# Kernel tuning notes

Measured on AMD Instinct MI355X. Metric: run time of the kernel, lower is better.

Reference implementation:

```python
import jax, jax.numpy as jnp
import numpy as np

RADIUS = 2  # scipy grey_opening 'size' -> flat 2x2 structuring element


def _grey_opening_2d(x, w=RADIUS):
    """Channel-wise grey opening matching scipy.ndimage.grey_opening(slice, size=w).

    scipy semantics for even size w=2:
      erosion window at i covers {i-1, i}  (filter centered, left-heavy)
      dilation window at i covers {i, i+1} (structuring element reflected)
    boundary mode 'reflect' in scipy.ndimage repeats the edge sample, which is
    jnp.pad mode='symmetric'.
    x: [B, C, H, W]
    """
    lo = w // 2          # left/top pad for erosion (=1 for w=2)
    hi = w - 1 - lo      # right/bottom pad for erosion (=0 for w=2)
    win = (1, 1, w, w)
    strides = (1, 1, 1, 1)
    # erosion: sliding-window min
    xe = jnp.pad(x, ((0, 0), (0, 0), (lo, hi), (lo, hi)), mode='symmetric')
    er = jax.lax.reduce_window(xe, jnp.array(jnp.inf, x.dtype), jax.lax.min,
                               win, strides, 'VALID')
    # dilation: sliding-window max with reflected (right-heavy) window
    xd = jnp.pad(er, ((0, 0), (0, 0), (hi, lo), (hi, lo)), mode='symmetric')
    return jax.lax.reduce_window(xd, jnp.array(-jnp.inf, x.dtype), jax.lax.max,
                                 win, strides, 'VALID')


def setup_inputs() -> dict:
    key = jax.random.key(0)
    labels = jax.random.uniform(key, (8, 16, 512, 512), dtype=jnp.float32)
    return {"labels": labels}


def reference(labels):
    # smooth labels are detached in the original (numpy round-trip + .detach())
    smooth = jax.lax.stop_gradient(_grey_opening_2d(labels))
    return jnp.mean((labels - smooth) ** 2)
```

## Files before the change

kernel.cpp:

```cpp
#include <hip/hip_runtime.h>


#define BLK 256
#define GRID 2048

__global__ __launch_bounds__(BLK) void opening_partial_kernel(
    const float* __restrict__ x, float* __restrict__ partial, int nGroups)
{
    float acc = 0.f;
    const int stride = gridDim.x * blockDim.x;
    for (int g = blockIdx.x * blockDim.x + threadIdx.x; g < nGroups; g += stride) {
        const int j = (g & 127) << 2;
        const int i = (g >> 7) & 511;
        const long long planeOff = ((long long)(g >> 16)) << 18;
        const float* r1 = x + planeOff + ((long long)i << 9);
        const float* r0 = (i > 0)   ? r1 - 512 : r1;
        const float* r2 = (i < 511) ? r1 + 512 : r1;

        const float4 v0 = *(const float4*)(r0 + j);
        const float4 v1 = *(const float4*)(r1 + j);
        const float4 v2 = *(const float4*)(r2 + j);
        const int jm = (j > 0)   ? j - 1 : 0;
        const int jp = (j < 508) ? j + 4 : 511;
        const float a0 = r0[jm], e0 = r0[jp];
        const float a1 = r1[jm], e1 = r1[jp];
        const float a2 = r2[jm], e2 = r2[jp];

        float m0[5] = { fminf(a0, v0.x), fminf(v0.x, v0.y), fminf(v0.y, v0.z),
                        fminf(v0.z, v0.w), fminf(v0.w, e0) };
        float m1[5] = { fminf(a1, v1.x), fminf(v1.x, v1.y), fminf(v1.y, v1.z),
                        fminf(v1.z, v1.w), fminf(v1.w, e1) };
        float m2[5] = { fminf(a2, v2.x), fminf(v2.x, v2.y), fminf(v2.y, v2.z),
                        fminf(v2.z, v2.w), fminf(v2.w, e2) };

        float erA[5], erB[5];
        const bool notBottom = (i < 511);
        #pragma unroll
        for (int c = 0; c < 5; ++c) {
            erA[c] = fminf(m0[c], m1[c]);
            const float inner = notBottom ? m1[c] : m0[c];
            erB[c] = fminf(inner, m2[c]);
        }

        const bool lastChunk = (j == 508);
        const float xv[4] = { v1.x, v1.y, v1.z, v1.w };
        #pragma unroll
        for (int k = 0; k < 4; ++k) {
            float eA2 = erA[k + 1], eB2 = erB[k + 1];
            if (lastChunk && k == 3) { eA2 = erA[3]; eB2 = erB[3]; }
            const float dl = fmaxf(fmaxf(erA[k], eA2), fmaxf(erB[k], eB2));
            const float d = xv[k] - dl;
            acc = fmaf(d, d, acc);
        }
    }

    #pragma unroll
    for (int off = 32; off > 0; off >>= 1)
        acc += __shfl_down(acc, off, 64);
    __shared__ float s[BLK / 64];
    if ((threadIdx.x & 63) == 0) s[threadIdx.x >> 6] = acc;
    __syncthreads();
    if (threadIdx.x == 0) {
        float t = 0.f;
        #pragma unroll
        for (int w = 0; w < BLK / 64; ++w) t += s[w];
        partial[blockIdx.x] = t;
    }
}

__global__ __launch_bounds__(256) void final_reduce_kernel(
    const float* __restrict__ partial, float* __restrict__ out, int n, float invN)
{
    float acc = 0.f;
    for (int idx = threadIdx.x; idx < n; idx += blockDim.x) acc += partial[idx];
    #pragma unroll
    for (int off = 32; off > 0; off >>= 1)
        acc += __shfl_down(acc, off, 64);
    __shared__ float s[4];
    if ((threadIdx.x & 63) == 0) s[threadIdx.x >> 6] = acc;
    __syncthreads();
    if (threadIdx.x == 0)
        out[0] = (s[0] + s[1] + s[2] + s[3]) * invN;
}

extern "C" void kernel_launch(void* const* d_in, const int* in_sizes, int n_in,
                              void* d_out, int out_size, void* d_ws, size_t ws_size,
                              hipStream_t stream) {
    const float* x = (const float*)d_in[0];
    float* out = (float*)d_out;
    float* ws = (float*)d_ws;
    const int N = in_sizes[0];
    const int nGroups = N >> 2;

    opening_partial_kernel<<<GRID, BLK, 0, stream>>>(x, ws, nGroups);
    final_reduce_kernel<<<1, 256, 0, stream>>>(ws, out, GRID, 1.0f / (float)N);
}
```

Before: 211.2 us.

## Process row strips per wavefront with rolling rows and shuffle halos

Each wavefront now covers a 16-row strip of one 512-wide plane, with each lane holding 8 columns. The kernel streams rows downward and keeps the previous row's horizontal minima and dilation results in registers, so each row is loaded about once instead of three times. Horizontal halo values come from neighbouring lanes through cross-lane shuffles instead of separate scalar loads. In exchange it adds a serial dependency down each strip, reloads one halo row per strip, and launches half as many blocks, which could reduce latency hiding.

```diff
diff --git a/kernel.cpp b/kernel.cpp
--- a/kernel.cpp
+++ b/kernel.cpp
@@ -2,55 +2,92 @@
 
 
 #define BLK 256
-#define GRID 2048
+#define R_STRIP 16
+#define GRID 1024
 
-__global__ __launch_bounds__(BLK) void opening_partial_kernel(
-    const float* __restrict__ x, float* __restrict__ partial, int nGroups)
+__device__ __forceinline__ void compute_h(float4 u0, float4 u1, int lane,
+                                          float h[9]) {
+    float xl = __shfl_up(u1.w, 1, 64);
+    float xr = __shfl_down(u0.x, 1, 64);
+    if (lane == 0)  xl = u0.x;
+    if (lane == 63) xr = u1.w;
+    h[0] = fminf(xl, u0.x);
+    h[1] = fminf(u0.x, u0.y);
+    h[2] = fminf(u0.y, u0.z);
+    h[3] = fminf(u0.z, u0.w);
+    h[4] = fminf(u0.w, u1.x);
+    h[5] = fminf(u1.x, u1.y);
+    h[6] = fminf(u1.y, u1.z);
+    h[7] = fminf(u1.z, u1.w);
+    h[8] = fminf(u1.w, xr);
+}
+
+__global__ __launch_bounds__(BLK) void opening_strip_kernel(
+    const float* __restrict__ x, float* __restrict__ partial, int nStrips)
 {
+    const int lane = threadIdx.x & 63;
+    const int waveId = blockIdx.x * (BLK / 64) + (threadIdx.x >> 6);
+    const int totalWaves = gridDim.x * (BLK / 64);
     float acc = 0.f;
-    const int stride = gridDim.x * blockDim.x;
-    for (int g = blockIdx.x * blockDim.x + threadIdx.x; g < nGroups; g += stride) {
-        const int j = (g & 127) << 2;
-        const int i = (g >> 7) & 511;
-        const long long planeOff = ((long long)(g >> 16)) << 18;
-        const float* r1 = x + planeOff + ((long long)i << 9);
-        const float* r0 = (i > 0)   ? r1 - 512 : r1;
-        const float* r2 = (i < 511) ? r1 + 512 : r1;
 
-        const float4 v0 = *(const float4*)(r0 + j);
-        const float4 v1 = *(const float4*)(r1 + j);
-        const float4 v2 = *(const float4*)(r2 + j);
-        const int jm = (j > 0)   ? j - 1 : 0;
-        const int jp = (j < 508) ? j + 4 : 511;
-        const float a0 = r0[jm], e0 = r0[jp];
-        const float a1 = r1[jm], e1 = r1[jp];
-        const float a2 = r2[jm], e2 = r2[jp];
+    for (int strip = waveId; strip < nStrips; strip += totalWaves) {
+        const int plane = strip >> 5;
+        const int rs = (strip & 31) * R_STRIP;
+        const int re = rs + R_STRIP - 1;
+        const int aEnd = (re < 511) ? re + 1 : 511;
+        const float* pl = x + (((long long)plane) << 18) + (lane << 3);
 
-        float m0[5] = { fminf(a0, v0.x), fminf(v0.x, v0.y), fminf(v0.y, v0.z),
-                        fminf(v0.z, v0.w), fminf(v0.w, e0) };
-        float m1[5] = { fminf(a1, v1.x), fminf(v1.x, v1.y), fminf(v1.y, v1.z),
-                        fminf(v1.z, v1.w), fminf(v1.w, e1) };
-        float m2[5] = { fminf(a2, v2.x), fminf(v2.x, v2.y), fminf(v2.y, v2.z),
-                        fminf(v2.z, v2.w), fminf(v2.w, e2) };
+        float hp[9], gp[8], xk[8];
 
-        float erA[5], erB[5];
-        const bool notBottom = (i < 511);
-        #pragma unroll
-        for (int c = 0; c < 5; ++c) {
-            erA[c] = fminf(m0[c], m1[c]);
-            const float inner = notBottom ? m1[c] : m0[c];
-            erB[c] = fminf(inner, m2[c]);
+        {
+            const int a0 = (rs > 0) ? rs - 1 : 0;
+            const float* rp = pl + ((long long)a0 << 9);
+            float4 u0 = *(const float4*)(rp);
+            float4 u1 = *(const float4*)(rp + 4);
+            compute_h(u0, u1, lane, hp);
+        }
+        float4 n0, n1;
+        {
+            const float* rp = pl + ((long long)rs << 9);
+            n0 = *(const float4*)(rp);
+            n1 = *(const float4*)(rp + 4);
         }
 
-        const bool lastChunk = (j == 508);
-        const float xv[4] = { v1.x, v1.y, v1.z, v1.w };
-        #pragma unroll
-        for (int k = 0; k < 4; ++k) {
-            float eA2 = erA[k + 1], eB2 = erB[k + 1];
-            if (lastChunk && k == 3) { eA2 = erA[3]; eB2 = erB[3]; }
-            const float dl = fmaxf(fmaxf(erA[k], eA2), fmaxf(erB[k], eB2));
-            const float d = xv[k] - dl;
-            acc = fmaf(d, d, acc);
+        for (int a = rs; a <= aEnd; ++a) {
+            const float4 u0 = n0, u1 = n1;
+            if (a < aEnd) {
+                const float* np = pl + ((long long)(a + 1) << 9);
+                n0 = *(const float4*)(np);
+                n1 = *(const float4*)(np + 4);
+            }
+            float hc[9], er[9], gc[8];
+            compute_h(u0, u1, lane, hc);
+            #pragma unroll
+            for (int c = 0; c < 9; ++c) er[c] = fminf(hp[c], hc[c]);
+            if (lane == 63) er[8] = er[7];
+            #pragma unroll
+            for (int c = 0; c < 8; ++c) gc[c] = fmaxf(er[c], er[c + 1]);
+
+            if (a > rs) {
+                #pragma unroll
+                for (int k = 0; k < 8; ++k) {
+                    const float d = xk[k] - fmaxf(gp[k], gc[k]);
+                    acc = fmaf(d, d, acc);
+                }
+            }
+            #pragma unroll
+            for (int c = 0; c < 9; ++c) hp[c] = hc[c];
+            #pragma unroll
+            for (int c = 0; c < 8; ++c) gp[c] = gc[c];
+            xk[0] = u0.x; xk[1] = u0.y; xk[2] = u0.z; xk[3] = u0.w;
+            xk[4] = u1.x; xk[5] = u1.y; xk[6] = u1.z; xk[7] = u1.w;
+        }
+        if (re == 511) {
+            #pragma unroll
+            for (int k = 0; k < 8; ++k) {
+                const float d = xk[k] - gp[k];
+                acc = fmaf(d, d, acc);
+            }
         }
     }
 
@@ -90,8 +127,8 @@
     float* out = (float*)d_out;
     float* ws = (float*)d_ws;
     const int N = in_sizes[0];
-    const int nGroups = N >> 2;
+    const int nStrips = (N >> 18) << 5;
 
-    opening_partial_kernel<<<GRID, BLK, 0, stream>>>(x, ws, nGroups);
+    opening_strip_kernel<<<GRID, BLK, 0, stream>>>(x, ws, nStrips);
     final_reduce_kernel<<<1, 256, 0, stream>>>(ws, out, GRID, 1.0f / (float)N);
 }
```

Result: faster. 188.4 us (-10.8%).
